# Kernel tuning notes

Measured on AMD Instinct MI355X. Metric: run time of the kernel, lower is better.

Reference implementation:

```python
import jax, jax.numpy as jnp
import numpy as np

# dims
B, NB, T, NC = 16, 55, 512, 8          # batch, filter bands, time steps, CSP comps
D, L, H, E, K, F, C = 512, 6, 8, 8, 2, 2048, 2  # embed, depth, heads, experts, top_k, d_ff, classes
DH = D // H
IN = NB * NC  # 440
EPS = 1e-5


def _ln(x, s, b):
    m = x.mean(-1, keepdims=True)
    v = ((x - m) ** 2).mean(-1, keepdims=True)
    return (x - m) / jnp.sqrt(v + EPS) * s + b


def setup_inputs() -> dict:
    key = jax.random.key(0)
    ks = iter(jax.random.split(key, 64))
    n = lambda shape, s=0.02: jax.random.normal(next(ks), shape, jnp.float32) * s
    inp = {
        "x": jax.random.normal(next(ks), (B, NB, T, NC), jnp.float32),
        # frontend
        "proj_w": n((IN, D)), "proj_b": jnp.zeros((D,), jnp.float32),
        "pos": n((1, T, D)),
        "ln_pre_s": jnp.ones((D,), jnp.float32), "ln_pre_b": jnp.zeros((D,), jnp.float32),
        # stacked transformer-block params [L, ...]
        "ln1_s": jnp.ones((L, D), jnp.float32), "ln1_b": jnp.zeros((L, D), jnp.float32),
        "wq": n((L, D, D)), "bq": jnp.zeros((L, D), jnp.float32),
        "wk": n((L, D, D)), "bk": jnp.zeros((L, D), jnp.float32),
        "wv": n((L, D, D)), "bv": jnp.zeros((L, D), jnp.float32),
        "wo": n((L, D, D)), "bo": jnp.zeros((L, D), jnp.float32),
        "ln2_s": jnp.ones((L, D), jnp.float32), "ln2_b": jnp.zeros((L, D), jnp.float32),
        "gate_w": n((L, D, E)),
        "e_w1": n((L, E, D, F)), "e_b1": jnp.zeros((L, E, F), jnp.float32),
        "e_w2": n((L, E, F, D)), "e_b2": jnp.zeros((L, E, D), jnp.float32),
        # classifier head
        "ln_f_s": jnp.ones((D,), jnp.float32), "ln_f_b": jnp.zeros((D,), jnp.float32),
        "head_w": n((D, C)), "head_b": jnp.zeros((C,), jnp.float32),
    }
    return inp


def _moe(h, gw, w1, b1, w2, b2):
    # h: [N, D]; top-K softmax-gated mixture of GELU-FFN experts + load-balance aux loss
    N = h.shape[0]
    probs = jax.nn.softmax(h @ gw, axis=-1)                  # [N, E]
    vals, idx = jax.lax.top_k(probs, K)                      # [N, K]
    w = vals / vals.sum(-1, keepdims=True)                   # renormalized top-k weights
    disp = jax.nn.one_hot(idx, E, dtype=h.dtype)             # [N, K, E]
    combine = (disp * w[..., None]).sum(1)                   # [N, E]
    y = jnp.zeros_like(h)
    for e in range(E):  # small fixed expert loop
        y = y + combine[:, e:e + 1] * (jax.nn.gelu(h @ w1[e] + b1[e]) @ w2[e] + b2[e])
    frac = disp.mean((0, 1)) * K                             # fraction of tokens routed to each expert
    aux = E * jnp.sum(frac * probs.mean(0))
    return y, aux


def reference(x, proj_w, proj_b, pos, ln_pre_s, ln_pre_b, ln1_s, ln1_b, wq, bq, wk, bk,
              wv, bv, wo, bo, ln2_s, ln2_b, gate_w, e_w1, e_b1, e_w2, e_b2,
              ln_f_s, ln_f_b, head_w, head_b):
    b, nb, t, nc = x.shape
    h = x.transpose(0, 2, 1, 3).reshape(b, t, nb * nc) @ proj_w + proj_b  # [B,T,D]
    h = _ln(h + pos[:, :t, :], ln_pre_s, ln_pre_b)
    scale = DH ** -0.5
    total_aux = jnp.float32(0.0)
    for l in range(L):
        # pre-LN multi-head self-attention
        a = _ln(h, ln1_s[l], ln1_b[l])
        q = (a @ wq[l] + bq[l]).reshape(b, t, H, DH)
        k = (a @ wk[l] + bk[l]).reshape(b, t, H, DH)
        v = (a @ wv[l] + bv[l]).reshape(b, t, H, DH)
        att = jax.nn.softmax(jnp.einsum('bqhd,bkhd->bhqk', q, k) * scale, axis=-1)
        o = jnp.einsum('bhqk,bkhd->bqhd', att, v).reshape(b, t, D) @ wo[l] + bo[l]
        h = h + o
        # pre-LN MoE FFN
        m = _ln(h, ln2_s[l], ln2_b[l]).reshape(b * t, D)
        y, aux = _moe(m, gate_w[l], e_w1[l], e_b1[l], e_w2[l], e_b2[l])
        h = h + y.reshape(b, t, D)
        total_aux = total_aux + aux
    pooled = h.mean(axis=1)                                   # [B, D]
    logits = _ln(pooled, ln_f_s, ln_f_b) @ head_w + head_b    # [B, C]
    return logits, total_aux
```

## Files before the change

### kernel.cpp

```cpp
#include <hip/hip_runtime.h>
#include <stdint.h>

typedef unsigned short u16;
typedef unsigned int   u32;
typedef short bh8 __attribute__((ext_vector_type(8)));
typedef float f4  __attribute__((ext_vector_type(4)));

#define NTOK    8192
#define PADROWS 17408
#define MAXTILES 136

__device__ __forceinline__ u16 f2bf(float f){
  u32 u = __float_as_uint(f);
  return (u16)((u + 0x7fffu + ((u>>16)&1u)) >> 16);
}
__device__ __forceinline__ float bf2f(u16 h){ return __uint_as_float(((u32)h)<<16); }
__device__ __forceinline__ u32 pk2(float a, float b){ return (u32)f2bf(a) | ((u32)f2bf(b)<<16); }
__device__ __forceinline__ float gelu_f(float x){
  float u = 0.7978845608028654f*(x + 0.044715f*x*x*x);
  float t = 1.f - 2.f/(__expf(2.f*u)+1.f);
  return 0.5f*x*(1.f+t);
}
__device__ __forceinline__ void gload_lds16(const void* g, void* l){
  __builtin_amdgcn_global_load_lds((const __attribute__((address_space(1))) u32*)g,
                                   (__attribute__((address_space(3))) u32*)l, 16, 0, 0);
}

__global__ __launch_bounds__(256) void xpose_k(const float* __restrict__ x, u16* __restrict__ xt){
  int idx = blockIdx.x*256 + threadIdx.x;
  const float* src = x + (size_t)idx*8;
  float4 a = *(const float4*)src;
  float4 b = *(const float4*)(src+4);
  int t  = idx & 511;
  int nb = (idx>>9) % 55;
  int bb = (idx>>9) / 55;
  uint4 u;
  u.x = pk2(a.x,a.y); u.y = pk2(a.z,a.w); u.z = pk2(b.x,b.y); u.w = pk2(b.z,b.w);
  *(uint4*)&xt[((size_t)(bb*512+t))*448 + nb*8] = u;
}

__device__ __forceinline__ void tile_xpose(const float* __restrict__ src, u16* __restrict__ dst,
                                           int Ksrc, int N, int Kdst, float (*tile)[65])
{
  int tid = threadIdx.x;
  int k0 = blockIdx.y*64, n0 = blockIdx.x*64;
  #pragma unroll
  for (int p=0;p<4;++p){
    int r = p*16 + (tid>>4);
    int c4 = (tid&15)*4;
    int k = k0 + r;
    float4 v = (k < Ksrc) ? *(const float4*)&src[(size_t)k*N + n0 + c4] : (float4){0.f,0.f,0.f,0.f};
    tile[r][c4]=v.x; tile[r][c4+1]=v.y; tile[r][c4+2]=v.z; tile[r][c4+3]=v.w;
  }
  __syncthreads();
  #pragma unroll
  for (int p=0;p<2;++p){
    int rn = p*32 + (tid>>3);
    int ck = (tid&7)*8;
    uint4 u;
    u.x = pk2(tile[ck+0][rn], tile[ck+1][rn]);
    u.y = pk2(tile[ck+2][rn], tile[ck+3][rn]);
    u.z = pk2(tile[ck+4][rn], tile[ck+5][rn]);
    u.w = pk2(tile[ck+6][rn], tile[ck+7][rn]);
    *(uint4*)&dst[(size_t)(n0+rn)*Kdst + k0 + ck] = u;
  }
}

__global__ __launch_bounds__(256) void wconv_k(const float* __restrict__ src, u16* __restrict__ dst,
                                               int Ksrc, int N, int Kdst){
  __shared__ float tile[64][65];
  src += (size_t)blockIdx.z*Ksrc*N;
  dst += (size_t)blockIdx.z*N*Kdst;
  tile_xpose(src, dst, Ksrc, N, Kdst, tile);
}

__global__ __launch_bounds__(256) void wconvqkvo_k(const float* __restrict__ wq, const float* __restrict__ wk,
    const float* __restrict__ wv, const float* __restrict__ wo,
    u16* __restrict__ qkvt, u16* __restrict__ wot)
{
  __shared__ float tile[64][65];
  int z = blockIdx.z;
  int l = z>>2, which = z&3;
  const float* src = ((which==0)? wq : (which==1)? wk : (which==2)? wv : wo) + (size_t)l*512*512;
  u16* dst = (which==3) ? wot + (size_t)l*512*512
                        : qkvt + (size_t)l*1536*512 + (size_t)which*512*512;
  tile_xpose(src, dst, 512, 512, 512, tile);
}

__global__ __launch_bounds__(256) void qkvb_k(const float* __restrict__ bq, const float* __restrict__ bk,
                                              const float* __restrict__ bv, float* __restrict__ qkvb){
  int idx = blockIdx.x*256 + threadIdx.x;
  int l = idx/1536, c = idx - l*1536;
  const float* s = (c<512)? bq : (c<1024)? bk : bv;
  qkvb[idx] = s[l*512 + (c&511)];
}

template<int MODE, bool GATHER>
__global__ __launch_bounds__(256) void gemm2_k(
    const u16* __restrict__ A, int lda,
    const u16* __restrict__ Bt, int ldb, int Ksteps,
    const float* __restrict__ biasBase,
    float* __restrict__ Cf, u16* __restrict__ Cb, int ldc,
    const int* __restrict__ tile_e, const int* __restrict__ toklist,
    const float* __restrict__ wlist, int expN)
{
  __shared__ __align__(16) u16 SMEM[24576];
  const int tid = threadIdx.x, lane = tid&63, w = tid>>6;
  const int wr = w>>1, wc = w&1;
  int nx = gridDim.x;
  int nwg = nx * gridDim.y;
  int lin = blockIdx.y*nx + blockIdx.x;
  int qq = nwg>>3, rr = nwg&7, xc = lin&7, oo = lin>>3;
  int wg = (xc<rr ? xc*(qq+1) : rr*(qq+1)+(xc-rr)*qq) + oo;
  int by = wg/nx, bx = wg - by*nx;
  const int n0 = bx*128, m0 = by*128;
  const u16* Bp = Bt;
  const float* bias = biasBase;
  if constexpr (MODE>=3){
    int e = tile_e[by];
    Bp   += (size_t)e*(size_t)expN*(size_t)ldb;
    bias += (size_t)e*(size_t)expN;
  }
  const u16* asrc0; const u16* asrc1; const u16* bsrc0; const u16* bsrc1;
  {
    int idx0 = tid, row0 = idx0>>2, sp0 = idx0&3, ks0 = sp0 ^ ((row0>>1)&3);
    int idx1 = 256+tid, row1 = idx1>>2, sp1 = idx1&3, ks1 = sp1 ^ ((row1>>1)&3);
    size_t ar0 = GATHER ? (size_t)toklist[m0+row0] : (size_t)(m0+row0);
    size_t ar1 = GATHER ? (size_t)toklist[m0+row1] : (size_t)(m0+row1);
    asrc0 = A + ar0*(size_t)lda + ks0*8;
    asrc1 = A + ar1*(size_t)lda + ks1*8;
    bsrc0 = Bp + (size_t)(n0+row0)*ldb + ks0*8;
    bsrc1 = Bp + (size_t)(n0+row1)*ldb + ks1*8;
  }
  f4 acc[4][4];
  #pragma unroll
  for (int i=0;i<4;++i)
    #pragma unroll
    for (int j=0;j<4;++j) acc[i][j] = (f4){0.f,0.f,0.f,0.f};

  auto STAGE = [&](int kt){
    u16* bufA = SMEM + (kt%3)*8192;
    u16* bufB = bufA + 4096;
    gload_lds16(asrc0 + (size_t)kt*32, &bufA[tid*8]);
    gload_lds16(asrc1 + (size_t)kt*32, &bufA[2048 + tid*8]);
    gload_lds16(bsrc0 + (size_t)kt*32, &bufB[tid*8]);
    gload_lds16(bsrc1 + (size_t)kt*32, &bufB[2048 + tid*8]);
  };

  STAGE(0);
  if (Ksteps > 1) STAGE(1);
  if (Ksteps > 2) STAGE(2);

  for (int kt=0; kt<Ksteps; ++kt){
    int rem = Ksteps - 1 - kt;
    if (rem >= 2)      asm volatile("s_waitcnt vmcnt(8)" ::: "memory");
    else if (rem == 1) asm volatile("s_waitcnt vmcnt(4)" ::: "memory");
    else               asm volatile("s_waitcnt vmcnt(0)" ::: "memory");
    __builtin_amdgcn_s_barrier();
    u16* bufA = SMEM + (kt%3)*8192;
    u16* bufB = bufA + 4096;
    bh8 af[4], bf[4];
    const int q = lane>>4;
    #pragma unroll
    for (int mf=0;mf<4;++mf){
      int r = wr*64 + mf*16 + (lane&15);
      af[mf] = *(const bh8*)&bufA[r*32 + (q ^ ((r>>1)&3))*8];
    }
    #pragma unroll
    for (int nf=0;nf<4;++nf){
      int r = wc*64 + nf*16 + (lane&15);
      bf[nf] = *(const bh8*)&bufB[r*32 + (q ^ ((r>>1)&3))*8];
    }
    asm volatile("s_waitcnt lgkmcnt(0)" ::: "memory");
    __builtin_amdgcn_sched_barrier(0);
    __builtin_amdgcn_s_barrier();
    __builtin_amdgcn_sched_barrier(0);
    if (kt+3 < Ksteps) STAGE(kt+3);
    #pragma unroll
    for (int mf=0;mf<4;++mf)
      #pragma unroll
      for (int nf=0;nf<4;++nf)
        acc[mf][nf] = __builtin_amdgcn_mfma_f32_16x16x32_bf16(af[mf], bf[nf], acc[mf][nf], 0, 0, 0);
  }
  if constexpr (MODE==1 || MODE==3 || MODE==4){
    __syncthreads();
    u16* Cs = SMEM;
    #pragma unroll
    for (int mf=0;mf<4;++mf){
      int row0 = wr*64 + mf*16 + (lane>>4)*4;
      float wl[4];
      if constexpr (MODE==4){
        #pragma unroll
        for (int r=0;r<4;++r) wl[r] = wlist[m0+row0+r];
      }
      #pragma unroll
      for (int nf=0;nf<4;++nf){
        f4 d = acc[mf][nf];
        int col = wc*64 + nf*16 + (lane&15);
        float bv = bias[n0+col];
        #pragma unroll
        for (int r=0;r<4;++r){
          float val = d[r] + bv;
          if constexpr (MODE==3) val = gelu_f(val);
          if constexpr (MODE==4) val = wl[r]*val;
          Cs[(row0+r)*136 + col] = f2bf(val);
        }
      }
    }
    __syncthreads();
    #pragma unroll
    for (int p=0;p<8;++p){
      int idx = p*256 + tid;
      int row = idx>>4, c4 = idx&15;
      bh8 v = *(const bh8*)&Cs[row*136 + c4*8];
      int mrow = m0 + row;
      if constexpr (MODE==1){
        int nc = n0 + c4*8;
        int slab = nc>>6, dh = nc&63;
        *(bh8*)&Cb[((size_t)slab*NTOK + (size_t)mrow)*64 + dh] = v;
      } else {
        *(bh8*)&Cb[(size_t)mrow*ldc + n0 + c4*8] = v;
      }
    }
  } else {
    #pragma unroll
    for (int mf=0;mf<4;++mf){
      #pragma unroll
      for (int nf=0;nf<4;++nf){
        f4 d = acc[mf][nf];
        int ncol = n0 + wc*64 + nf*16 + (lane&15);
        float bv = bias[ncol];
        #pragma unroll
        for (int r=0;r<4;++r){
          int mrow = m0 + wr*64 + mf*16 + (lane>>4)*4 + r;
          float val = d[r] + bv;
          if constexpr (MODE==0){
            Cf[(size_t)mrow*ldc + ncol] = val;
          } else {
            Cf[(size_t)mrow*ldc + ncol] += val;
          }
        }
      }
    }
  }
}

template<bool ADDPOS, bool OUTF32>
__global__ __launch_bounds__(256) void ln_k(const float* __restrict__ X, const float* __restrict__ pos,
    const float* __restrict__ sc, const float* __restrict__ bi,
    float* __restrict__ outF, u16* __restrict__ outB)
{
  int tid=threadIdx.x, lane=tid&63, w=tid>>6;
  int row = blockIdx.x*4 + w;
  const float* xr = X + (size_t)row*512 + lane*8;
  float x[8];
  float4 v0 = *(const float4*)xr;
  float4 v1 = *(const float4*)(xr+4);
  x[0]=v0.x;x[1]=v0.y;x[2]=v0.z;x[3]=v0.w;x[4]=v1.x;x[5]=v1.y;x[6]=v1.z;x[7]=v1.w;
  if constexpr (ADDPOS){
    const float* pr = pos + (size_t)(row&511)*512 + lane*8;
    float4 p0 = *(const float4*)pr, p1 = *(const float4*)(pr+4);
    x[0]+=p0.x;x[1]+=p0.y;x[2]+=p0.z;x[3]+=p0.w;x[4]+=p1.x;x[5]+=p1.y;x[6]+=p1.z;x[7]+=p1.w;
  }
  float sm=0.f, sq=0.f;
  #pragma unroll
  for (int i=0;i<8;++i){ sm+=x[i]; sq+=x[i]*x[i]; }
  #pragma unroll
  for (int mk=1; mk<64; mk<<=1){ sm += __shfl_xor(sm, mk); sq += __shfl_xor(sq, mk); }
  float mean = sm*(1.f/512.f);
  float var  = sq*(1.f/512.f) - mean*mean;
  float rstd = rsqrtf(var + 1e-5f);
  int d0 = lane*8;
  float4 s0 = *(const float4*)(sc+d0), s1 = *(const float4*)(sc+d0+4);
  float4 b0 = *(const float4*)(bi+d0), b1 = *(const float4*)(bi+d0+4);
  float y[8];
  y[0]=(x[0]-mean)*rstd*s0.x+b0.x; y[1]=(x[1]-mean)*rstd*s0.y+b0.y;
  y[2]=(x[2]-mean)*rstd*s0.z+b0.z; y[3]=(x[3]-mean)*rstd*s0.w+b0.w;
  y[4]=(x[4]-mean)*rstd*s1.x+b1.x; y[5]=(x[5]-mean)*rstd*s1.y+b1.y;
  y[6]=(x[6]-mean)*rstd*s1.z+b1.z; y[7]=(x[7]-mean)*rstd*s1.w+b1.w;
  if constexpr (OUTF32){
    float4 o0 = {y[0],y[1],y[2],y[3]}, o1 = {y[4],y[5],y[6],y[7]};
    *(float4*)(outF + (size_t)row*512 + d0)     = o0;
    *(float4*)(outF + (size_t)row*512 + d0 + 4) = o1;
  } else {
    uint4 u; u.x=pk2(y[0],y[1]); u.y=pk2(y[2],y[3]); u.z=pk2(y[4],y[5]); u.w=pk2(y[6],y[7]);
    *(uint4*)&outB[(size_t)row*512 + d0] = u;
  }
}

__global__ __launch_bounds__(256) void gatherln_k(float* __restrict__ h,
    const u16* __restrict__ yb, const int* __restrict__ t2pos,
    const float* __restrict__ sc, const float* __restrict__ bi, u16* __restrict__ outB)
{
  int tid=threadIdx.x, lane=tid&63, w=tid>>6;
  int row = blockIdx.x*4 + w;
  float* hp = h + (size_t)row*512 + lane*8;
  float4 v0 = *(float4*)hp, v1 = *(float4*)(hp+4);
  int p0 = t2pos[2*row], p1 = t2pos[2*row+1];
  uint4 ya = *(const uint4*)&yb[(size_t)p0*512 + lane*8];
  uint4 yv = *(const uint4*)&yb[(size_t)p1*512 + lane*8];
  float x[8];
  x[0]=v0.x + bf2f((u16)(ya.x&0xffff)) + bf2f((u16)(yv.x&0xffff));
  x[1]=v0.y + bf2f((u16)(ya.x>>16))    + bf2f((u16)(yv.x>>16));
  x[2]=v0.z + bf2f((u16)(ya.y&0xffff)) + bf2f((u16)(yv.y&0xffff));
  x[3]=v0.w + bf2f((u16)(ya.y>>16))    + bf2f((u16)(yv.y>>16));
  x[4]=v1.x + bf2f((u16)(ya.z&0xffff)) + bf2f((u16)(yv.z&0xffff));
  x[5]=v1.y + bf2f((u16)(ya.z>>16))    + bf2f((u16)(yv.z>>16));
  x[6]=v1.z + bf2f((u16)(ya.w&0xffff)) + bf2f((u16)(yv.w&0xffff));
  x[7]=v1.w + bf2f((u16)(ya.w>>16))    + bf2f((u16)(yv.w>>16));
  float4 o0 = {x[0],x[1],x[2],x[3]}, o1 = {x[4],x[5],x[6],x[7]};
  *(float4*)hp = o0; *(float4*)(hp+4) = o1;
  float sm=0.f, sq=0.f;
  #pragma unroll
  for (int i=0;i<8;++i){ sm+=x[i]; sq+=x[i]*x[i]; }
  #pragma unroll
  for (int mk=1; mk<64; mk<<=1){ sm += __shfl_xor(sm, mk); sq += __shfl_xor(sq, mk); }
  float mean = sm*(1.f/512.f);
  float rstd = rsqrtf(sq*(1.f/512.f) - mean*mean + 1e-5f);
  int d0 = lane*8;
  float4 s0 = *(const float4*)(sc+d0), s1 = *(const float4*)(sc+d0+4);
  float4 b0 = *(const float4*)(bi+d0), b1 = *(const float4*)(bi+d0+4);
  float y[8];
  y[0]=(x[0]-mean)*rstd*s0.x+b0.x; y[1]=(x[1]-mean)*rstd*s0.y+b0.y;
  y[2]=(x[2]-mean)*rstd*s0.z+b0.z; y[3]=(x[3]-mean)*rstd*s0.w+b0.w;
  y[4]=(x[4]-mean)*rstd*s1.x+b1.x; y[5]=(x[5]-mean)*rstd*s1.y+b1.y;
  y[6]=(x[6]-mean)*rstd*s1.z+b1.z; y[7]=(x[7]-mean)*rstd*s1.w+b1.w;
  uint4 u; u.x=pk2(y[0],y[1]); u.y=pk2(y[2],y[3]); u.z=pk2(y[4],y[5]); u.w=pk2(y[6],y[7]);
  *(uint4*)&outB[(size_t)row*512 + d0] = u;
}

__global__ __launch_bounds__(256) void attn_k(const u16* __restrict__ QKV, u16* __restrict__ Og)
{
  __shared__ __align__(16) u16 VT[2][64*72];
  __shared__ __align__(16) u16 PS[4][16*72];
  int tid=threadIdx.x, lane=tid&63, w=tid>>6;
  int qt=blockIdx.x, hh=blockIdx.y, bb=blockIdx.z;
  const u16* Qh = QKV + ((size_t)hh     *NTOK + (size_t)bb*512)*64;
  const u16* Kh = QKV + ((size_t)(8+hh) *NTOK + (size_t)bb*512)*64;
  const u16* Vh = QKV + ((size_t)(16+hh)*NTOK + (size_t)bb*512)*64;
  size_t obase = (size_t)bb*512*512 + (size_t)hh*64;
  int qrow0 = qt*64 + w*16;
  bh8 qf[2];
  #pragma unroll
  for (int kf=0;kf<2;++kf)
    qf[kf] = *(const bh8*)&Qh[ (size_t)(qrow0 + (lane&15))*64 + kf*32 + (lane>>4)*8 ];
  f4 oacc[4];
  #pragma unroll
  for (int i=0;i<4;++i) oacc[i] = (f4){0.f,0.f,0.f,0.f};
  float mrun[4] = {-1e30f,-1e30f,-1e30f,-1e30f};
  float lrun[4] = {0.f,0.f,0.f,0.f};
  const float scale = 0.125f;

  for (int kt=0; kt<8; ++kt){
    const int buf = kt&1;
    #pragma unroll
    for (int r2=0;r2<2;++r2){
      int idx = r2*256 + tid;
      int dhg = idx&7;
      int dh0 = dhg*8, key = idx>>3;
      uint4 raw = *(const uint4*)&Vh[ (size_t)(kt*64+key)*64 + dh0 ];
      int kx = key ^ (dhg<<3);
      u32 rw[4] = {raw.x, raw.y, raw.z, raw.w};
      #pragma unroll
      for (int j=0;j<4;++j){
        VT[buf][(dh0+2*j  )*72 + kx] = (u16)(rw[j]&0xffff);
        VT[buf][(dh0+2*j+1)*72 + kx] = (u16)(rw[j]>>16);
      }
    }
    f4 s[4];
    #pragma unroll
    for (int nf=0;nf<4;++nf){
      size_t krow = (size_t)(kt*64+nf*16+(lane&15))*64 + (lane>>4)*8;
      bh8 k0 = *(const bh8*)&Kh[krow];
      bh8 k1 = *(const bh8*)&Kh[krow+32];
      f4 z = (f4){0.f,0.f,0.f,0.f};
      z = __builtin_amdgcn_mfma_f32_16x16x32_bf16(qf[0], k0, z, 0,0,0);
      z = __builtin_amdgcn_mfma_f32_16x16x32_bf16(qf[1], k1, z, 0,0,0);
      s[nf] = z;
    }
    float pe[4][4];
    #pragma unroll
    for (int r=0;r<4;++r){
      float sv0=s[0][r]*scale, sv1=s[1][r]*scale, sv2=s[2][r]*scale, sv3=s[3][r]*scale;
      float mt = fmaxf(fmaxf(sv0,sv1), fmaxf(sv2,sv3));
      #pragma unroll
      for (int mk=1; mk<16; mk<<=1) mt = fmaxf(mt, __shfl_xor(mt, mk));
      float mn = fmaxf(mrun[r], mt);
      float sf = __expf(mrun[r]-mn);
      float p0=__expf(sv0-mn), p1=__expf(sv1-mn), p2=__expf(sv2-mn), p3=__expf(sv3-mn);
      pe[0][r]=p0; pe[1][r]=p1; pe[2][r]=p2; pe[3][r]=p3;
      float rs = p0+p1+p2+p3;
      #pragma unroll
      for (int mk=1; mk<16; mk<<=1) rs += __shfl_xor(rs, mk);
      lrun[r] = lrun[r]*sf + rs;
      mrun[r] = mn;
      #pragma unroll
      for (int df=0;df<4;++df) oacc[df][r] *= sf;
    }
    #pragma unroll
    for (int nf=0;nf<4;++nf)
      #pragma unroll
      for (int r=0;r<4;++r)
        PS[w][ ((lane>>4)*4+r)*72 + nf*16 + (lane&15) ] = f2bf(pe[nf][r]);
    __syncthreads();
    #pragma unroll
    for (int ks=0;ks<2;++ks){
      bh8 pa = *(const bh8*)&PS[w][ (lane&15)*72 + ks*32 + (lane>>4)*8 ];
      #pragma unroll
      for (int df=0;df<4;++df){
        int dh = df*16 + (lane&15);
        int sgrp = (dh>>3)&7;
        bh8 vb = *(const bh8*)&VT[buf][ dh*72 + ((ks*4 + (lane>>4)) ^ sgrp)*8 ];
        oacc[df] = __builtin_amdgcn_mfma_f32_16x16x32_bf16(pa, vb, oacc[df], 0,0,0);
      }
    }
  }
  #pragma unroll
  for (int df=0;df<4;++df)
    #pragma unroll
    for (int r=0;r<4;++r){
      int qr = qrow0 + (lane>>4)*4 + r;
      float ov = oacc[df][r] / lrun[r];
      Og[ obase + (size_t)qr*512 + df*16 + (lane&15) ] = f2bf(ov);
    }
}

__global__ __launch_bounds__(256) void lnroute_k(const float* __restrict__ h,
    const float* __restrict__ sc, const float* __restrict__ bi, u16* __restrict__ outB,
    const float* __restrict__ gw,
    float* __restrict__ psum, int* __restrict__ cnt, int* __restrict__ t2e, float* __restrict__ t2w)
{
  __shared__ float ps[8]; __shared__ int cs[8];
  int tid=threadIdx.x, lane=tid&63, w=tid>>6;
  if (tid<8){ ps[tid]=0.f; cs[tid]=0; }
  __syncthreads();
  int d0 = lane*8;
  float4 s0 = *(const float4*)(sc+d0), s1 = *(const float4*)(sc+d0+4);
  float4 b0 = *(const float4*)(bi+d0), b1 = *(const float4*)(bi+d0+4);
  for (int it=0; it<4; ++it){
    int t = blockIdx.x*16 + w*4 + it;
    const float* xr = h + (size_t)t*512 + d0;
    float x[8];
    float4 v0 = *(const float4*)xr, v1 = *(const float4*)(xr+4);
    x[0]=v0.x;x[1]=v0.y;x[2]=v0.z;x[3]=v0.w;x[4]=v1.x;x[5]=v1.y;x[6]=v1.z;x[7]=v1.w;
    float sm=0.f, sq=0.f;
    #pragma unroll
    for (int i=0;i<8;++i){ sm+=x[i]; sq+=x[i]*x[i]; }
    #pragma unroll
    for (int mk=1; mk<64; mk<<=1){ sm += __shfl_xor(sm, mk); sq += __shfl_xor(sq, mk); }
    float mean = sm*(1.f/512.f);
    float rstd = rsqrtf(sq*(1.f/512.f) - mean*mean + 1e-5f);
    float y[8];
    y[0]=(x[0]-mean)*rstd*s0.x+b0.x; y[1]=(x[1]-mean)*rstd*s0.y+b0.y;
    y[2]=(x[2]-mean)*rstd*s0.z+b0.z; y[3]=(x[3]-mean)*rstd*s0.w+b0.w;
    y[4]=(x[4]-mean)*rstd*s1.x+b1.x; y[5]=(x[5]-mean)*rstd*s1.y+b1.y;
    y[6]=(x[6]-mean)*rstd*s1.z+b1.z; y[7]=(x[7]-mean)*rstd*s1.w+b1.w;
    uint4 u; u.x=pk2(y[0],y[1]); u.y=pk2(y[2],y[3]); u.z=pk2(y[4],y[5]); u.w=pk2(y[6],y[7]);
    *(uint4*)&outB[(size_t)t*512 + d0] = u;
    float acc[8] = {0,0,0,0,0,0,0,0};
    #pragma unroll
    for (int j=0;j<8;++j){
      const float* g = gw + (size_t)(d0+j)*8;
      float4 g0 = *(const float4*)g, g1 = *(const float4*)(g+4);
      acc[0]+=y[j]*g0.x; acc[1]+=y[j]*g0.y; acc[2]+=y[j]*g0.z; acc[3]+=y[j]*g0.w;
      acc[4]+=y[j]*g1.x; acc[5]+=y[j]*g1.y; acc[6]+=y[j]*g1.z; acc[7]+=y[j]*g1.w;
    }
    #pragma unroll
    for (int mk=1; mk<64; mk<<=1)
      #pragma unroll
      for (int e=0;e<8;++e) acc[e] += __shfl_xor(acc[e], mk);
    if (lane==0){
      float mx=acc[0];
      #pragma unroll
      for (int e=1;e<8;++e) mx = fmaxf(mx, acc[e]);
      float pe[8], tot=0.f;
      #pragma unroll
      for (int e=0;e<8;++e){ pe[e]=__expf(acc[e]-mx); tot+=pe[e]; }
      float inv = 1.f/tot;
      #pragma unroll
      for (int e=0;e<8;++e) pe[e]*=inv;
      int e0=0; float v0e=pe[0];
      #pragma unroll
      for (int e=1;e<8;++e) if (pe[e]>v0e){ v0e=pe[e]; e0=e; }
      int e1=-1; float v1e=-1.f;
      #pragma unroll
      for (int e=0;e<8;++e) if (e!=e0 && pe[e]>v1e){ v1e=pe[e]; e1=e; }
      float invw = 1.f/(v0e+v1e);
      t2e[2*t]=e0; t2w[2*t]=v0e*invw; t2e[2*t+1]=e1; t2w[2*t+1]=v1e*invw;
      #pragma unroll
      for (int e=0;e<8;++e) atomicAdd(&ps[e], pe[e]);
      atomicAdd(&cs[e0],1); atomicAdd(&cs[e1],1);
    }
  }
  __syncthreads();
  if (tid<8){ atomicAdd(&psum[tid], ps[tid]); atomicAdd(&cnt[tid], cs[tid]); }
}

__global__ __launch_bounds__(256) void offsets_k(const int* __restrict__ cnt, const float* __restrict__ psum,
    int* __restrict__ offs, int* __restrict__ fill, int* __restrict__ tile_e,
    int* __restrict__ toklist, float* __restrict__ wlist, float* __restrict__ auxp)
{
  int tid = threadIdx.x, b = blockIdx.x;
  int i = b*256 + tid;
  if (i < PADROWS){ toklist[i]=0; wlist[i]=0.f; }
  if (b==0){
    if (tid==0){
      int off=0; float auxl=0.f;
      for (int e=0;e<8;++e){
        offs[e] = off;
        int reg = (cnt[e]+127)&~127;
        int t0 = off>>7, t1 = (off+reg)>>7;
        for (int t=t0;t<t1;++t) tile_e[t]=e;
        off += reg;
        auxl += ((float)cnt[e]*(1.f/8192.f)) * (psum[e]*(1.f/8192.f));
      }
      for (int t=off>>7; t<MAXTILES; ++t) tile_e[t]=0;
      auxp[0] += 8.f*auxl;
    }
    if (tid<8) fill[tid]=0;
  }
}

__global__ __launch_bounds__(256) void scatter_k(const int* __restrict__ t2e, const float* __restrict__ t2w,
    const int* __restrict__ offs, int* __restrict__ fill,
    int* __restrict__ toklist, float* __restrict__ wlist, int* __restrict__ t2pos)
{
  int t = blockIdx.x*256 + threadIdx.x;
  #pragma unroll
  for (int kk=0;kk<2;++kk){
    int e = t2e[2*t+kk];
    int p = atomicAdd(&fill[e], 1);
    int i = offs[e] + p;
    toklist[i] = t; wlist[i] = t2w[2*t+kk]; t2pos[2*t+kk] = i;
  }
}

__global__ __launch_bounds__(256) void gather_k(float* __restrict__ h, const u16* __restrict__ yb,
                                                const int* __restrict__ t2pos)
{
  int tid = threadIdx.x;
  int t = blockIdx.x*4 + (tid>>6);
  int lane = tid&63;
  int p0 = t2pos[2*t], p1 = t2pos[2*t+1];
  uint4 a = *(const uint4*)&yb[(size_t)p0*512 + lane*8];
  uint4 b = *(const uint4*)&yb[(size_t)p1*512 + lane*8];
  float* hp = h + (size_t)t*512 + lane*8;
  float4 h0 = *(float4*)hp, h1 = *(float4*)(hp+4);
  h0.x += bf2f((u16)(a.x&0xffff)) + bf2f((u16)(b.x&0xffff));
  h0.y += bf2f((u16)(a.x>>16))    + bf2f((u16)(b.x>>16));
  h0.z += bf2f((u16)(a.y&0xffff)) + bf2f((u16)(b.y&0xffff));
  h0.w += bf2f((u16)(a.y>>16))    + bf2f((u16)(b.y>>16));
  h1.x += bf2f((u16)(a.z&0xffff)) + bf2f((u16)(b.z&0xffff));
  h1.y += bf2f((u16)(a.z>>16))    + bf2f((u16)(b.z>>16));
  h1.z += bf2f((u16)(a.w&0xffff)) + bf2f((u16)(b.w&0xffff));
  h1.w += bf2f((u16)(a.w>>16))    + bf2f((u16)(b.w>>16));
  *(float4*)hp = h0; *(float4*)(hp+4) = h1;
}

__global__ __launch_bounds__(256) void pool_k(const float* __restrict__ h, float* __restrict__ pooled){
  int idx = blockIdx.x*256 + threadIdx.x;
  int bb = idx>>9, d = idx&511;
  const float* p = h + (size_t)bb*512*512 + d;
  float s=0.f;
  for (int t=0;t<512;++t) s += p[(size_t)t*512];
  pooled[idx] = s*(1.f/512.f);
}

__global__ __launch_bounds__(256) void head_k(const float* __restrict__ pooled,
    const float* __restrict__ sc, const float* __restrict__ bi,
    const float* __restrict__ hw, const float* __restrict__ hb,
    const float* __restrict__ auxp, float* __restrict__ out)
{
  int tid=threadIdx.x, lane=tid&63, w=tid>>6;
  for (int i=0;i<4;++i){
    int row = w*4+i;
    const float* xr = pooled + (size_t)row*512 + lane*8;
    float x[8];
    float4 v0 = *(const float4*)xr, v1 = *(const float4*)(xr+4);
    x[0]=v0.x;x[1]=v0.y;x[2]=v0.z;x[3]=v0.w;x[4]=v1.x;x[5]=v1.y;x[6]=v1.z;x[7]=v1.w;
    float sm=0.f, sq=0.f;
    #pragma unroll
    for (int j=0;j<8;++j){ sm+=x[j]; sq+=x[j]*x[j]; }
    #pragma unroll
    for (int mk=1; mk<64; mk<<=1){ sm += __shfl_xor(sm, mk); sq += __shfl_xor(sq, mk); }
    float mean = sm*(1.f/512.f);
    float rstd = rsqrtf(sq*(1.f/512.f) - mean*mean + 1e-5f);
    int d0 = lane*8;
    float c0=0.f, c1=0.f;
    #pragma unroll
    for (int j=0;j<8;++j){
      float yv = (x[j]-mean)*rstd*sc[d0+j] + bi[d0+j];
      c0 += yv*hw[(d0+j)*2]; c1 += yv*hw[(d0+j)*2+1];
    }
    #pragma unroll
    for (int mk=1; mk<64; mk<<=1){ c0 += __shfl_xor(c0, mk); c1 += __shfl_xor(c1, mk); }
    if (lane==0){ out[row*2+0] = c0 + hb[0]; out[row*2+1] = c1 + hb[1]; }
  }
  if (tid==0) out[32] = auxp[0];
}

extern "C" void kernel_launch(void* const* d_in, const int* in_sizes, int n_in,
                              void* d_out, int out_size, void* d_ws, size_t ws_size,
                              hipStream_t stream)
{
  (void)in_sizes; (void)n_in; (void)out_size; (void)ws_size;
  const float* x      = (const float*)d_in[0];
  const float* proj_w = (const float*)d_in[1];
  const float* proj_b = (const float*)d_in[2];
  const float* pos    = (const float*)d_in[3];
  const float* ln_pre_s=(const float*)d_in[4];
  const float* ln_pre_b=(const float*)d_in[5];
  const float* ln1_s  = (const float*)d_in[6];
  const float* ln1_b  = (const float*)d_in[7];
  const float* wq     = (const float*)d_in[8];
  const float* bq     = (const float*)d_in[9];
  const float* wk     = (const float*)d_in[10];
  const float* bk     = (const float*)d_in[11];
  const float* wv     = (const float*)d_in[12];
  const float* bv     = (const float*)d_in[13];
  const float* wo     = (const float*)d_in[14];
  const float* bo     = (const float*)d_in[15];
  const float* ln2_s  = (const float*)d_in[16];
  const float* ln2_b  = (const float*)d_in[17];
  const float* gate_w = (const float*)d_in[18];
  const float* e_w1   = (const float*)d_in[19];
  const float* e_b1   = (const float*)d_in[20];
  const float* e_w2   = (const float*)d_in[21];
  const float* e_b2   = (const float*)d_in[22];
  const float* ln_f_s = (const float*)d_in[23];
  const float* ln_f_b = (const float*)d_in[24];
  const float* head_w = (const float*)d_in[25];
  const float* head_b = (const float*)d_in[26];

  char* base = (char*)d_ws;
  size_t off = 0;
  auto carve = [&](size_t bytes)->char*{
    char* r = base + off; off += (bytes + 255) & ~(size_t)255; return r;
  };
  u16*   xt      = (u16*)  carve((size_t)8192*448*2);
  float* h       = (float*)carve((size_t)8192*512*4);
  u16*   a       = (u16*)  carve((size_t)8192*512*2);
  u16*   qkv     = (u16*)  carve((size_t)8192*1536*2);
  u16*   ob      = (u16*)  carve((size_t)8192*512*2);
  u16*   hidden  = (u16*)  carve((size_t)PADROWS*2048*2);
  u16*   ybuf    = (u16*)  carve((size_t)PADROWS*512*2);
  u16*   projt   = (u16*)  carve((size_t)512*448*2);
  u16*   qkvt    = (u16*)  carve((size_t)6*1536*512*2);
  u16*   wot     = (u16*)  carve((size_t)6*512*512*2);
  u16*   w1t     = (u16*)  carve((size_t)6*8*2048*512*2);
  u16*   w2t     = (u16*)  carve((size_t)6*8*512*2048*2);
  float* qkvb    = (float*)carve((size_t)6*1536*4);
  int*   toklist = (int*)  carve(PADROWS*4);
  float* wlist   = (float*)carve(PADROWS*4);
  int*   tile_e  = (int*)  carve(256*4);
  int*   rcntA   = (int*)  carve(6*16*4);
  int*   fill    = (int*)  carve(64);
  int*   offs    = (int*)  carve(64);
  int*   t2e     = (int*)  carve(16384*4);
  float* t2w     = (float*)carve(16384*4);
  int*   t2pos   = (int*)  carve(16384*4);
  float* pooled  = (float*)carve(8192*4);
  float* auxp    = (float*)carve(256);

  hipMemsetAsync(xt, 0, (size_t)8192*448*2, stream);
  hipMemsetAsync(rcntA, 0, 6*16*4, stream);
  hipMemsetAsync(auxp, 0, 4, stream);

  xpose_k<<<1760, 256, 0, stream>>>(x, xt);
  wconv_k<<<dim3(8,7,1), 256, 0, stream>>>(proj_w, projt, 440, 512, 448);
  wconvqkvo_k<<<dim3(8,8,24), 256, 0, stream>>>(wq, wk, wv, wo, qkvt, wot);
  wconv_k<<<dim3(32,8,48), 256, 0, stream>>>(e_w1, w1t, 512, 2048, 512);
  wconv_k<<<dim3(8,32,48), 256, 0, stream>>>(e_w2, w2t, 2048, 512, 2048);
  qkvb_k<<<36, 256, 0, stream>>>(bq, bk, bv, qkvb);
  gemm2_k<0,false><<<dim3(4,64), 256, 0, stream>>>(xt, 448, projt, 448, 14, proj_b,
      h, nullptr, 512, nullptr, nullptr, nullptr, 0);
  ln_k<true,true><<<2048, 256, 0, stream>>>(h, pos, ln_pre_s, ln_pre_b, h, nullptr);

  for (int l=0; l<6; ++l){
    int*   cnt  = rcntA + l*16;
    float* psum = (float*)(cnt + 8);
    if (l == 0)
      ln_k<false,false><<<2048, 256, 0, stream>>>(h, nullptr, ln1_s, ln1_b, nullptr, a);
    else
      gatherln_k<<<2048, 256, 0, stream>>>(h, ybuf, t2pos,
          ln1_s+(size_t)l*512, ln1_b+(size_t)l*512, a);
    gemm2_k<1,false><<<dim3(12,64), 256, 0, stream>>>(a, 512, qkvt+(size_t)l*1536*512, 512, 16,
        qkvb+(size_t)l*1536, nullptr, qkv, 1536, nullptr, nullptr, nullptr, 0);
    attn_k<<<dim3(8,8,16), 256, 0, stream>>>(qkv, ob);
    gemm2_k<2,false><<<dim3(4,64), 256, 0, stream>>>(ob, 512, wot+(size_t)l*512*512, 512, 16,
        bo+(size_t)l*512, h, nullptr, 512, nullptr, nullptr, nullptr, 0);
    lnroute_k<<<512, 256, 0, stream>>>(h, ln2_s+(size_t)l*512, ln2_b+(size_t)l*512, a,
        gate_w+(size_t)l*512*8, psum, cnt, t2e, t2w);
    offsets_k<<<68, 256, 0, stream>>>(cnt, psum, offs, fill, tile_e, toklist, wlist, auxp);
    scatter_k<<<32, 256, 0, stream>>>(t2e, t2w, offs, fill, toklist, wlist, t2pos);
    gemm2_k<3,true ><<<dim3(16,MAXTILES), 256, 0, stream>>>(a, 512, w1t+(size_t)l*8*2048*512, 512, 16,
        e_b1 + (size_t)l*8*2048, nullptr, hidden, 2048, tile_e, toklist, wlist, 2048);
    gemm2_k<4,false><<<dim3(4,MAXTILES), 256, 0, stream>>>(hidden, 2048, w2t+(size_t)l*8*512*2048, 2048, 64,
        e_b2 + (size_t)l*8*512, nullptr, ybuf, 512, tile_e, nullptr, wlist, 512);
  }

  gather_k<<<2048, 256, 0, stream>>>(h, ybuf, t2pos);
  pool_k<<<32, 256, 0, stream>>>(h, pooled);
  head_k<<<1, 256, 0, stream>>>(pooled, ln_f_s, ln_f_b, head_w, head_b, auxp, (float*)d_out);
}
```

Before: 2.097 ms.

## Add 128x256 tile GEMM kernel for QKV and MoE expert projections

Introduces gemm3_k, which computes a 128x256 output tile per workgroup. Each of the four waves owns a 64-column strip across all 128 rows, giving 8x4 MFMA accumulators per wave. It is used for the QKV projection and both MoE expert GEMMs, which halves the grid width and reuses each A tile across twice as many columns. The original gemm2_k keeps only the fp32 store paths. The trade-off is more LDS (72KB) and more accumulator registers per wave, which lowers occupancy, and fewer workgroups per launch.

```diff
diff --git a/kernel.cpp b/kernel.cpp
--- a/kernel.cpp
+++ b/kernel.cpp
@@ -116,11 +116,6 @@
   const int n0 = bx*128, m0 = by*128;
   const u16* Bp = Bt;
   const float* bias = biasBase;
-  if constexpr (MODE>=3){
-    int e = tile_e[by];
-    Bp   += (size_t)e*(size_t)expN*(size_t)ldb;
-    bias += (size_t)e*(size_t)expN;
-  }
   const u16* asrc0; const u16* asrc1; const u16* bsrc0; const u16* bsrc1;
   {
     int idx0 = tid, row0 = idx0>>2, sp0 = idx0&3, ks0 = sp0 ^ ((row0>>1)&3);
@@ -146,7 +141,6 @@
     gload_lds16(bsrc0 + (size_t)kt*32, &bufB[tid*8]);
     gload_lds16(bsrc1 + (size_t)kt*32, &bufB[2048 + tid*8]);
   };
-
   STAGE(0);
   if (Ksteps > 1) STAGE(1);
   if (Ksteps > 2) STAGE(2);
@@ -182,65 +176,154 @@
       for (int nf=0;nf<4;++nf)
         acc[mf][nf] = __builtin_amdgcn_mfma_f32_16x16x32_bf16(af[mf], bf[nf], acc[mf][nf], 0, 0, 0);
   }
-  if constexpr (MODE==1 || MODE==3 || MODE==4){
-    __syncthreads();
-    u16* Cs = SMEM;
-    #pragma unroll
-    for (int mf=0;mf<4;++mf){
-      int row0 = wr*64 + mf*16 + (lane>>4)*4;
-      float wl[4];
-      if constexpr (MODE==4){
-        #pragma unroll
-        for (int r=0;r<4;++r) wl[r] = wlist[m0+row0+r];
-      }
-      #pragma unroll
-      for (int nf=0;nf<4;++nf){
-        f4 d = acc[mf][nf];
-        int col = wc*64 + nf*16 + (lane&15);
-        float bv = bias[n0+col];
-        #pragma unroll
-        for (int r=0;r<4;++r){
-          float val = d[r] + bv;
-          if constexpr (MODE==3) val = gelu_f(val);
-          if constexpr (MODE==4) val = wl[r]*val;
-          Cs[(row0+r)*136 + col] = f2bf(val);
+  #pragma unroll
+  for (int mf=0;mf<4;++mf){
+    #pragma unroll
+    for (int nf=0;nf<4;++nf){
+      f4 d = acc[mf][nf];
+      int ncol = n0 + wc*64 + nf*16 + (lane&15);
+      float bv = bias[ncol];
+      #pragma unroll
+      for (int r=0;r<4;++r){
+        int mrow = m0 + wr*64 + mf*16 + (lane>>4)*4 + r;
+        float val = d[r] + bv;
+        if constexpr (MODE==0){
+          Cf[(size_t)mrow*ldc + ncol] = val;
+        } else {
+          Cf[(size_t)mrow*ldc + ncol] += val;
         }
       }
     }
-    __syncthreads();
-    #pragma unroll
-    for (int p=0;p<8;++p){
-      int idx = p*256 + tid;
-      int row = idx>>4, c4 = idx&15;
-      bh8 v = *(const bh8*)&Cs[row*136 + c4*8];
-      int mrow = m0 + row;
-      if constexpr (MODE==1){
-        int nc = n0 + c4*8;
-        int slab = nc>>6, dh = nc&63;
-        *(bh8*)&Cb[((size_t)slab*NTOK + (size_t)mrow)*64 + dh] = v;
-      } else {
-        *(bh8*)&Cb[(size_t)mrow*ldc + n0 + c4*8] = v;
+  }
+}
+
+template<int MODE, bool GATHER>
+__global__ __launch_bounds__(256) void gemm3_k(
+    const u16* __restrict__ A, int lda,
+    const u16* __restrict__ Bt, int ldb, int Ksteps,
+    const float* __restrict__ biasBase,
+    u16* __restrict__ Cb, int ldc,
+    const int* __restrict__ tile_e, const int* __restrict__ toklist,
+    const float* __restrict__ wlist, int expN)
+{
+  __shared__ __align__(16) u16 SMEM[36864];
+  const int tid = threadIdx.x, lane = tid&63, w = tid>>6;
+  int nx = gridDim.x;
+  int nwg = nx * gridDim.y;
+  int lin = blockIdx.y*nx + blockIdx.x;
+  int qq = nwg>>3, rr = nwg&7, xc = lin&7, oo = lin>>3;
+  int wg = (xc<rr ? xc*(qq+1) : rr*(qq+1)+(xc-rr)*qq) + oo;
+  int by = wg/nx, bx = wg - by*nx;
+  const int n0 = bx*256, m0 = by*128;
+  const u16* Bp = Bt;
+  const float* bias = biasBase;
+  if constexpr (MODE>=3){
+    int e = tile_e[by];
+    Bp   += (size_t)e*(size_t)expN*(size_t)ldb;
+    bias += (size_t)e*(size_t)expN;
+  }
+  const u16* asrc0; const u16* asrc1;
+  const u16* bsrcp[4];
+  {
+    int row0 = tid>>2, sp0 = tid&3, ks0 = sp0 ^ ((row0>>1)&3);
+    int idx1 = 256+tid, row1 = idx1>>2, sp1 = idx1&3, ks1 = sp1 ^ ((row1>>1)&3);
+    size_t ar0 = GATHER ? (size_t)toklist[m0+row0] : (size_t)(m0+row0);
+    size_t ar1 = GATHER ? (size_t)toklist[m0+row1] : (size_t)(m0+row1);
+    asrc0 = A + ar0*(size_t)lda + ks0*8;
+    asrc1 = A + ar1*(size_t)lda + ks1*8;
+    #pragma unroll
+    for (int p=0;p<4;++p){
+      int idx = p*256 + tid, row = idx>>2, sp = idx&3, ks = sp ^ ((row>>1)&3);
+      bsrcp[p] = Bp + (size_t)(n0+row)*ldb + ks*8;
+    }
+  }
+  f4 acc[8][4];
+  #pragma unroll
+  for (int i=0;i<8;++i)
+    #pragma unroll
+    for (int j=0;j<4;++j) acc[i][j] = (f4){0.f,0.f,0.f,0.f};
+
+  auto STAGE = [&](int kt){
+    u16* bufA = SMEM + (kt%3)*12288;
+    u16* bufB = bufA + 4096;
+    gload_lds16(asrc0 + (size_t)kt*32, &bufA[tid*8]);
+    gload_lds16(asrc1 + (size_t)kt*32, &bufA[2048 + tid*8]);
+    #pragma unroll
+    for (int p=0;p<4;++p)
+      gload_lds16(bsrcp[p] + (size_t)kt*32, &bufB[(p*256+tid)*8]);
+  };
+  STAGE(0);
+  if (Ksteps > 1) STAGE(1);
+  if (Ksteps > 2) STAGE(2);
+
+  for (int kt=0; kt<Ksteps; ++kt){
+    int rem = Ksteps - 1 - kt;
+    if (rem >= 2)      asm volatile("s_waitcnt vmcnt(12)" ::: "memory");
+    else if (rem == 1) asm volatile("s_waitcnt vmcnt(6)" ::: "memory");
+    else               asm volatile("s_waitcnt vmcnt(0)" ::: "memory");
+    __builtin_amdgcn_s_barrier();
+    u16* bufA = SMEM + (kt%3)*12288;
+    u16* bufB = bufA + 4096;
+    bh8 af[8], bf[4];
+    const int q = lane>>4;
+    #pragma unroll
+    for (int mf=0;mf<8;++mf){
+      int r = mf*16 + (lane&15);
+      af[mf] = *(const bh8*)&bufA[r*32 + (q ^ ((r>>1)&3))*8];
+    }
+    #pragma unroll
+    for (int nf=0;nf<4;++nf){
+      int r = w*64 + nf*16 + (lane&15);
+      bf[nf] = *(const bh8*)&bufB[r*32 + (q ^ ((r>>1)&3))*8];
+    }
+    asm volatile("s_waitcnt lgkmcnt(0)" ::: "memory");
+    __builtin_amdgcn_sched_barrier(0);
+    __builtin_amdgcn_s_barrier();
+    __builtin_amdgcn_sched_barrier(0);
+    if (kt+3 < Ksteps) STAGE(kt+3);
+    #pragma unroll
+    for (int mf=0;mf<8;++mf)
+      #pragma unroll
+      for (int nf=0;nf<4;++nf)
+        acc[mf][nf] = __builtin_amdgcn_mfma_f32_16x16x32_bf16(af[mf], bf[nf], acc[mf][nf], 0, 0, 0);
+  }
+  __syncthreads();
+  u16* Cs = SMEM;
+  #pragma unroll
+  for (int mf=0;mf<8;++mf){
+    int row0 = mf*16 + (lane>>4)*4;
+    float wl[4];
+    if constexpr (MODE==4){
+      #pragma unroll
+      for (int r=0;r<4;++r) wl[r] = wlist[m0+row0+r];
+    }
+    #pragma unroll
+    for (int nf=0;nf<4;++nf){
+      f4 d = acc[mf][nf];
+      int col = w*64 + nf*16 + (lane&15);
+      float bv = bias[n0+col];
+      #pragma unroll
+      for (int r=0;r<4;++r){
+        float val = d[r] + bv;
+        if constexpr (MODE==3) val = gelu_f(val);
+        if constexpr (MODE==4) val = wl[r]*val;
+        Cs[(row0+r)*264 + col] = f2bf(val);
       }
     }
-  } else {
-    #pragma unroll
-    for (int mf=0;mf<4;++mf){
-      #pragma unroll
-      for (int nf=0;nf<4;++nf){
-        f4 d = acc[mf][nf];
-        int ncol = n0 + wc*64 + nf*16 + (lane&15);
-        float bv = bias[ncol];
-        #pragma unroll
-        for (int r=0;r<4;++r){
-          int mrow = m0 + wr*64 + mf*16 + (lane>>4)*4 + r;
-          float val = d[r] + bv;
-          if constexpr (MODE==0){
-            Cf[(size_t)mrow*ldc + ncol] = val;
-          } else {
-            Cf[(size_t)mrow*ldc + ncol] += val;
-          }
-        }
-      }
+  }
+  __syncthreads();
+  #pragma unroll
+  for (int p=0;p<16;++p){
+    int idx = p*256 + tid;
+    int row = idx>>5, c4 = idx&31;
+    bh8 v = *(const bh8*)&Cs[row*264 + c4*8];
+    int mrow = m0 + row;
+    if constexpr (MODE==1){
+      int nc = n0 + c4*8;
+      int slab = nc>>6, dh = nc&63;
+      *(bh8*)&Cb[((size_t)slab*NTOK + (size_t)mrow)*64 + dh] = v;
+    } else {
+      *(bh8*)&Cb[(size_t)mrow*ldc + n0 + c4*8] = v;
     }
   }
 }
@@ -684,8 +767,8 @@
     else
       gatherln_k<<<2048, 256, 0, stream>>>(h, ybuf, t2pos,
           ln1_s+(size_t)l*512, ln1_b+(size_t)l*512, a);
-    gemm2_k<1,false><<<dim3(12,64), 256, 0, stream>>>(a, 512, qkvt+(size_t)l*1536*512, 512, 16,
-        qkvb+(size_t)l*1536, nullptr, qkv, 1536, nullptr, nullptr, nullptr, 0);
+    gemm3_k<1,false><<<dim3(6,64), 256, 0, stream>>>(a, 512, qkvt+(size_t)l*1536*512, 512, 16,
+        qkvb+(size_t)l*1536, qkv, 1536, nullptr, nullptr, nullptr, 0);
     attn_k<<<dim3(8,8,16), 256, 0, stream>>>(qkv, ob);
     gemm2_k<2,false><<<dim3(4,64), 256, 0, stream>>>(ob, 512, wot+(size_t)l*512*512, 512, 16,
         bo+(size_t)l*512, h, nullptr, 512, nullptr, nullptr, nullptr, 0);
@@ -693,10 +776,10 @@
         gate_w+(size_t)l*512*8, psum, cnt, t2e, t2w);
     offsets_k<<<68, 256, 0, stream>>>(cnt, psum, offs, fill, tile_e, toklist, wlist, auxp);
     scatter_k<<<32, 256, 0, stream>>>(t2e, t2w, offs, fill, toklist, wlist, t2pos);
-    gemm2_k<3,true ><<<dim3(16,MAXTILES), 256, 0, stream>>>(a, 512, w1t+(size_t)l*8*2048*512, 512, 16,
-        e_b1 + (size_t)l*8*2048, nullptr, hidden, 2048, tile_e, toklist, wlist, 2048);
-    gemm2_k<4,false><<<dim3(4,MAXTILES), 256, 0, stream>>>(hidden, 2048, w2t+(size_t)l*8*512*2048, 2048, 64,
-        e_b2 + (size_t)l*8*512, nullptr, ybuf, 512, tile_e, nullptr, wlist, 512);
+    gemm3_k<3,true ><<<dim3(8,MAXTILES), 256, 0, stream>>>(a, 512, w1t+(size_t)l*8*2048*512, 512, 16,
+        e_b1 + (size_t)l*8*2048, hidden, 2048, tile_e, toklist, wlist, 2048);
+    gemm3_k<4,false><<<dim3(2,MAXTILES), 256, 0, stream>>>(hidden, 2048, w2t+(size_t)l*8*512*2048, 2048, 64,
+        e_b2 + (size_t)l*8*512, ybuf, 512, tile_e, nullptr, wlist, 512);
   }
 
   gather_k<<<2048, 256, 0, stream>>>(h, ybuf, t2pos);
```

After: 2.498 ms. 19.2% more time.
